# Kernel tuning notes

Measured on AMD Instinct MI355X. Metric: run time of the kernel, lower is better.

## Reference

```python
import jax, jax.numpy as jnp
import numpy as np
import math

B, S, D_MODEL, H, CLIP = 4, 1024, 1024, 16, 16
HEAD_DIM = D_MODEL // H
NEG = -1e6


def setup_inputs() -> dict:
    key = jax.random.key(0)
    ks = jax.random.split(key, 10)
    scale = 1.0 / math.sqrt(D_MODEL)
    return {
        "queries": jax.random.normal(ks[0], (B, S, D_MODEL), jnp.float32),
        "keys": jax.random.normal(ks[1], (B, S, D_MODEL), jnp.float32),
        "values": jax.random.normal(ks[2], (B, S, D_MODEL), jnp.float32),
        "valid_lens": jax.random.randint(ks[3], (B,), 1, S + 1),
        "Wq": jax.random.normal(ks[4], (D_MODEL, D_MODEL), jnp.float32) * scale,
        "Wk": jax.random.normal(ks[5], (D_MODEL, D_MODEL), jnp.float32) * scale,
        "Wv": jax.random.normal(ks[6], (D_MODEL, D_MODEL), jnp.float32) * scale,
        "Wo": jax.random.normal(ks[7], (D_MODEL, D_MODEL), jnp.float32) * scale,
        "Ek": jax.random.normal(ks[8], (2 * CLIP + 1, HEAD_DIM), jnp.float32),
        "Ev": jax.random.normal(ks[9], (2 * CLIP + 1, HEAD_DIM), jnp.float32),
    }


def _split_heads(x):
    # [B, S, D] -> [B*H, S, head_dim]
    b, s, _ = x.shape
    return x.reshape(b, s, H, HEAD_DIM).transpose(0, 2, 1, 3).reshape(b * H, s, HEAD_DIM)


def reference(queries, keys, values, valid_lens, Wq, Wk, Wv, Wo, Ek, Ev):
    q = _split_heads(queries @ Wq.T)  # [BH, S, d]
    k = _split_heads(keys @ Wk.T)
    v = _split_heads(values @ Wv.T)

    # relative-position tables, shared across batch and heads: [Sq, Sk, d]
    rng = jnp.arange(S)
    dist = jnp.clip(rng[None, :] - rng[:, None], -CLIP, CLIP) + CLIP
    pos_k = Ek[dist]
    pos_v = Ev[dist]

    scores = jnp.einsum('bqd,bkd->bqk', q, k) + jnp.einsum('bqd,qkd->bqk', q, pos_k)
    scores = scores / math.sqrt(HEAD_DIM)

    vl = jnp.repeat(valid_lens, H)  # [B*H]
    mask = jnp.arange(S)[None, None, :] < vl[:, None, None]
    attn = jax.nn.softmax(jnp.where(mask, scores, NEG), axis=-1)

    out = jnp.einsum('bqk,bkd->bqd', attn, v) + jnp.einsum('bqk,qkd->bqd', attn, pos_v)

    # merge heads: [B*H, S, d] -> [B, S, D]
    out = out.reshape(B, H, S, HEAD_DIM).transpose(0, 2, 1, 3).reshape(B, S, D_MODEL)
    return out @ Wo.T
```

## Files before the change

kernel.cpp:

```cpp
#include <hip/hip_runtime.h>


typedef __attribute__((ext_vector_type(8))) short short8;
typedef __attribute__((ext_vector_type(4))) float floatx4;

__device__ __forceinline__ unsigned short f2bf(float f) {
  union { float f; unsigned u; } v; v.f = f;
  return (unsigned short)((v.u + 0x7fffu + ((v.u >> 16) & 1u)) >> 16);
}
__device__ __forceinline__ unsigned packbf(float lo, float hi) {
  return ((unsigned)f2bf(hi) << 16) | (unsigned)f2bf(lo);
}

__device__ __forceinline__ void gld16(const void* g, void* l) {
  __builtin_amdgcn_global_load_lds(
      (const __attribute__((address_space(1))) unsigned*)g,
      (__attribute__((address_space(3))) unsigned*)l, 16, 0, 0);
}

#define WS_XQ  ((size_t)0)
#define WS_XK  ((size_t)4194304)
#define WS_XV  ((size_t)8388608)
#define WS_W   ((size_t)12582912)
#define WS_EKB ((size_t)16777216)
#define WS_EVT ((size_t)16781312)
#define WS_QB  ((size_t)16785408)
#define WS_KB  ((size_t)20979712)
#define WS_VT  ((size_t)25174016)
#define WS_OB  ((size_t)0)

__global__ __launch_bounds__(256) void convert_all_kernel(
    const float* __restrict__ q, const float* __restrict__ k,
    const float* __restrict__ v,
    const float* __restrict__ wq, const float* __restrict__ wk,
    const float* __restrict__ wv, const float* __restrict__ wo,
    const float* __restrict__ Ek, const float* __restrict__ Ev,
    const int* __restrict__ valid_lens, unsigned short* __restrict__ ws) {
  int z = blockIdx.z;
  if (z < 3) {
    const float* src = z == 0 ? q : (z == 1 ? k : v);
    unsigned short* dst = ws + (size_t)z * 4194304;
    size_t i = ((size_t)blockIdx.x * 256 + threadIdx.x) * 8;
    if (z > 0) {
      int b = (int)(i >> 20), s = (int)((i >> 10) & 1023);
      if (s >= valid_lens[b]) return;
    }
    float4 a = *(const float4*)(src + i);
    float4 bb = *(const float4*)(src + i + 4);
    uint4 o = { packbf(a.x, a.y), packbf(a.z, a.w), packbf(bb.x, bb.y), packbf(bb.z, bb.w) };
    *(uint4*)(dst + i) = o;
  } else if (z < 7) {
    if (blockIdx.x >= 512) return;
    const float* src = (z == 3) ? wq : (z == 4 ? wk : (z == 5 ? wv : wo));
    unsigned short* dst = ws + WS_W + (size_t)(z - 3) * 1048576;
    size_t i = ((size_t)blockIdx.x * 256 + threadIdx.x) * 8;
    float4 a = *(const float4*)(src + i);
    float4 bb = *(const float4*)(src + i + 4);
    uint4 o = { packbf(a.x, a.y), packbf(a.z, a.w), packbf(bb.x, bb.y), packbf(bb.z, bb.w) };
    *(uint4*)(dst + i) = o;
  } else {
    if (blockIdx.x >= 4) return;
    int gid = blockIdx.x * 256 + threadIdx.x;
    unsigned short* ekb = ws + WS_EKB;
    int i0 = gid * 8;
    unsigned short vals[8];
#pragma unroll
    for (int u = 0; u < 8; u++) {
      int i = i0 + u;
      if (i < 4096) {
        int t = i >> 6, d = i & 63;
        vals[u] = (t < 33) ? f2bf(Ek[t * 64 + d]) : (unsigned short)0;
      } else {
        int j = i - 4096;
        int d = j >> 6, t = j & 63;
        vals[u] = (t < 33) ? f2bf(Ev[t * 64 + d]) : (unsigned short)0;
      }
    }
    *(uint4*)(ekb + i0) = *(uint4*)vals;
  }
}

__device__ __forceinline__ void gemm128_body(
    const unsigned short* __restrict__ A, const unsigned short* __restrict__ W,
    unsigned short* __restrict__ Cb, float* __restrict__ Cf, int mode, float scale) {
  __shared__ unsigned short sA[128 * 32];
  __shared__ unsigned short sB[128 * 32];
  const int tid = threadIdx.x, wave = tid >> 6, lane = tid & 63;
  const int lr = lane & 15, lq = lane >> 4;
  const int wr = wave >> 1, wc = wave & 1;
  const int m0 = blockIdx.y * 128, n0 = blockIdx.x * 128;
  const int srow = lane >> 2, scol = (lane & 3) * 8;

  const unsigned short* gA0 = A + (size_t)(m0 + wave * 16 + srow) * 1024 + scol;
  const unsigned short* gA1 = gA0 + (size_t)64 * 1024;
  const unsigned short* gB0 = W + (size_t)(n0 + wave * 16 + srow) * 1024 + scol;
  const unsigned short* gB1 = gB0 + (size_t)64 * 1024;
  unsigned short* lA0 = sA + wave * 512;  unsigned short* lA1 = lA0 + 2048;
  unsigned short* lB0 = sB + wave * 512;  unsigned short* lB1 = lB0 + 2048;

  floatx4 acc[4][4];
#pragma unroll
  for (int mi = 0; mi < 4; mi++)
#pragma unroll
    for (int ni = 0; ni < 4; ni++) acc[mi][ni] = (floatx4){0.f, 0.f, 0.f, 0.f};

  for (int k0 = 0; k0 < 1024; k0 += 32) {
    gld16(gA0 + k0, lA0); gld16(gA1 + k0, lA1);
    gld16(gB0 + k0, lB0); gld16(gB1 + k0, lB1);
    __syncthreads();
    short8 af[4], bf[4];
#pragma unroll
    for (int mi = 0; mi < 4; mi++)
      af[mi] = *(const short8*)(sA + (wr * 64 + mi * 16 + lr) * 32 + lq * 8);
#pragma unroll
    for (int ni = 0; ni < 4; ni++)
      bf[ni] = *(const short8*)(sB + (wc * 64 + ni * 16 + lr) * 32 + lq * 8);
#pragma unroll
    for (int mi = 0; mi < 4; mi++)
#pragma unroll
      for (int ni = 0; ni < 4; ni++)
        acc[mi][ni] = __builtin_amdgcn_mfma_f32_16x16x32_bf16(af[mi], bf[ni], acc[mi][ni], 0, 0, 0);
    __syncthreads();
  }

  if (mode == 2) {
#pragma unroll
    for (int mi = 0; mi < 4; mi++)
#pragma unroll
      for (int ni = 0; ni < 4; ni++) {
        int col = n0 + wc * 64 + ni * 16 + lr;
        int h = col >> 6, d = col & 63;
        int rowg = m0 + wr * 64 + mi * 16 + lq * 4;
        int b = rowg >> 10, s = rowg & 1023;
        uint2 pk;
        pk.x = packbf(acc[mi][ni][0], acc[mi][ni][1]);
        pk.y = packbf(acc[mi][ni][2], acc[mi][ni][3]);
        *(uint2*)(Cb + ((size_t)((b * 16 + h) * 64 + d) << 10) + s) = pk;
      }
  } else if (mode == 3) {
#pragma unroll
    for (int mi = 0; mi < 4; mi++)
#pragma unroll
      for (int ni = 0; ni < 4; ni++)
#pragma unroll
        for (int r = 0; r < 4; r++) {
          int row = m0 + wr * 64 + mi * 16 + lq * 4 + r;
          int col = n0 + wc * 64 + ni * 16 + lr;
          Cf[(size_t)row * 1024 + col] = acc[mi][ni][r];
        }
  } else {
#pragma unroll
    for (int mi = 0; mi < 4; mi++)
#pragma unroll
      for (int ni = 0; ni < 4; ni++)
#pragma unroll
        for (int r = 0; r < 4; r++) {
          int row = m0 + wr * 64 + mi * 16 + lq * 4 + r;
          int col = n0 + wc * 64 + ni * 16 + lr;
          Cb[(size_t)row * 1024 + col] = f2bf(acc[mi][ni][r] * scale);
        }
  }
}

__global__ __launch_bounds__(256, 3) void proj_qkv_kernel(
    unsigned short* __restrict__ ws, const int* __restrict__ valid_lens) {
  int z = blockIdx.z;
  if (z > 0) {
    int m0 = blockIdx.y * 128;
    if ((m0 & 1023) >= valid_lens[m0 >> 10]) return;
  }
  const unsigned short* A = ws + (size_t)z * 4194304;
  const unsigned short* W = ws + WS_W + (size_t)z * 1048576;
  unsigned short* Cb = (z == 0) ? ws + WS_QB : (z == 1 ? ws + WS_KB : ws + WS_VT);
  int mode = (z == 2) ? 2 : (z == 0 ? 0 : 1);
  float scale = (z == 0) ? 0.125f : 1.0f;
  gemm128_body(A, W, Cb, nullptr, mode, scale);
}

__global__ __launch_bounds__(256, 3) void out_proj_kernel(
    const unsigned short* __restrict__ Ob, const unsigned short* __restrict__ Wo,
    float* __restrict__ out) {
  gemm128_body(Ob, Wo, nullptr, out, 3, 1.f);
}

__global__ __launch_bounds__(64, 3) void attn_rpr_kernel(
    const unsigned short* __restrict__ Qb, const unsigned short* __restrict__ Kb,
    const unsigned short* __restrict__ Vt, const int* __restrict__ valid_lens,
    const unsigned short* __restrict__ Ekb, const unsigned short* __restrict__ Evtb,
    unsigned short* __restrict__ Ob) {
  __shared__ unsigned short sP[16 * 72];
  __shared__ float sQE[16 * 34];
  __shared__ float sW[16 * 34];

  const int lane = threadIdx.x;
  const int lr = lane & 15, lq = lane >> 4;
  const int qx = blockIdx.x, bh = blockIdx.y;
  const int b = bh >> 4;
  const int vlen = valid_lens[b];
  const int i0 = qx * 16;
  const int colh = (bh & 15) * 64;
  const size_t bat = (size_t)b * 1024 * 1024;
  const int rbase = lq * 4;

  for (int i = lane; i < 16 * 34; i += 64) sW[i] = 0.f;

  const unsigned short* gQ = Qb + bat + (size_t)(i0 + lr) * 1024 + colh + lq * 8;
  short8 aq0 = *(const short8*)(gQ);
  short8 aq1 = *(const short8*)(gQ + 32);

#pragma unroll
  for (int ni = 0; ni < 3; ni++) {
    floatx4 aqe = (floatx4){0.f, 0.f, 0.f, 0.f};
    short8 be0 = *(const short8*)(Ekb + (ni * 16 + lr) * 64 + lq * 8);
    short8 be1 = *(const short8*)(Ekb + (ni * 16 + lr) * 64 + 32 + lq * 8);
    aqe = __builtin_amdgcn_mfma_f32_16x16x32_bf16(aq0, be0, aqe, 0, 0, 0);
    aqe = __builtin_amdgcn_mfma_f32_16x16x32_bf16(aq1, be1, aqe, 0, 0, 0);
    int t = ni * 16 + lr;
    if (t < 33)
#pragma unroll
      for (int r = 0; r < 4; r++) sQE[(rbase + r) * 34 + t] = aqe[r];
  }

  floatx4 acc_o[4];
#pragma unroll
  for (int nd = 0; nd < 4; nd++) acc_o[nd] = (floatx4){0.f, 0.f, 0.f, 0.f};
  float rs0[4] = {0.f, 0.f, 0.f, 0.f};
  float rs32[4] = {0.f, 0.f, 0.f, 0.f};

  const int vcl = vlen < 1024 ? vlen : 1024;
  const int kt_max = (vcl + 63) >> 6;

  const unsigned short* gK = Kb + bat + colh;
  const unsigned short* gV = Vt + ((size_t)bh * 64) * 1024;

  for (int kt = 0; kt < kt_max; kt++) {
    const int j0 = kt * 64;

    short8 bk[4][2], bv[4][2];
#pragma unroll
    for (int ni = 0; ni < 4; ni++) {
      const unsigned short* p = gK + (size_t)(j0 + ni * 16 + lr) * 1024 + lq * 8;
      bk[ni][0] = *(const short8*)(p);
      bk[ni][1] = *(const short8*)(p + 32);
    }
#pragma unroll
    for (int nd = 0; nd < 4; nd++) {
      const unsigned short* p = gV + (size_t)(nd * 16 + lr) * 1024 + j0 + lq * 8;
      bv[nd][0] = *(const short8*)(p);
      bv[nd][1] = *(const short8*)(p + 32);
    }

    floatx4 accs[4];
#pragma unroll
    for (int ni = 0; ni < 4; ni++) {
      accs[ni] = (floatx4){0.f, 0.f, 0.f, 0.f};
      accs[ni] = __builtin_amdgcn_mfma_f32_16x16x32_bf16(aq0, bk[ni][0], accs[ni], 0, 0, 0);
      accs[ni] = __builtin_amdgcn_mfma_f32_16x16x32_bf16(aq1, bk[ni][1], accs[ni], 0, 0, 0);
    }

    const bool general = (j0 > i0 - 79) && (j0 < i0 + 31);
    if (!general) {
      const bool hi = (j0 >= i0 + 31);
      const int tconst = hi ? 32 : 0;
      float qe[4];
#pragma unroll
      for (int r = 0; r < 4; r++) qe[r] = sQE[(rbase + r) * 34 + tconst];
#pragma unroll
      for (int ni = 0; ni < 4; ni++)
#pragma unroll
        for (int r = 0; r < 4; r++) {
          int j_g = j0 + ni * 16 + lr;
          float pv = (j_g < vlen) ? __expf(accs[ni][r] + qe[r]) : 0.f;
          if (hi) rs32[r] += pv; else rs0[r] += pv;
          sP[(rbase + r) * 72 + ni * 16 + lr] = f2bf(pv);
        }
    } else {
#pragma unroll
      for (int ni = 0; ni < 4; ni++)
#pragma unroll
        for (int r = 0; r < 4; r++) {
          int i_g = i0 + rbase + r;
          int j_g = j0 + ni * 16 + lr;
          int dd = j_g - i_g; dd = dd < -16 ? -16 : (dd > 16 ? 16 : dd);
          int t = dd + 16;
          float pv = (j_g < vlen) ? __expf(accs[ni][r] + sQE[(rbase + r) * 34 + t]) : 0.f;
          atomicAdd(&sW[(rbase + r) * 34 + t], pv);
          sP[(rbase + r) * 72 + ni * 16 + lr] = f2bf(pv);
        }
    }

    short8 ap0 = *(const short8*)(sP + lr * 72 + lq * 8);
    short8 ap1 = *(const short8*)(sP + lr * 72 + 32 + lq * 8);
#pragma unroll
    for (int nd = 0; nd < 4; nd++) {
      acc_o[nd] = __builtin_amdgcn_mfma_f32_16x16x32_bf16(ap0, bv[nd][0], acc_o[nd], 0, 0, 0);
      acc_o[nd] = __builtin_amdgcn_mfma_f32_16x16x32_bf16(ap1, bv[nd][1], acc_o[nd], 0, 0, 0);
    }
  }

#pragma unroll
  for (int x = 1; x < 16; x <<= 1)
#pragma unroll
    for (int r = 0; r < 4; r++) {
      rs0[r] += __shfl_xor(rs0[r], x, 64);
      rs32[r] += __shfl_xor(rs32[r], x, 64);
    }
  if (lr == 0)
#pragma unroll
    for (int r = 0; r < 4; r++) {
      sW[(rbase + r) * 34 + 0] += rs0[r];
      sW[(rbase + r) * 34 + 32] += rs32[r];
    }

  {
    int row = lane >> 2;
    int c0 = (lane & 3) * 16;
    unsigned* sP32 = (unsigned*)sP;
#pragma unroll
    for (int q = 0; q < 8; q++) {
      int t0 = c0 + 2 * q, t1 = t0 + 1;
      float w0 = (t0 < 33) ? sW[row * 34 + t0] : 0.f;
      float w1 = (t1 < 33) ? sW[row * 34 + t1] : 0.f;
      sP32[row * 36 + (c0 >> 1) + q] = packbf(w0, w1);
    }
  }
  {
    short8 aw0 = *(const short8*)(sP + lr * 72 + lq * 8);
    short8 aw1 = *(const short8*)(sP + lr * 72 + 32 + lq * 8);
#pragma unroll
    for (int nd = 0; nd < 4; nd++) {
      short8 be0 = *(const short8*)(Evtb + (nd * 16 + lr) * 64 + lq * 8);
      short8 be1 = *(const short8*)(Evtb + (nd * 16 + lr) * 64 + 32 + lq * 8);
      acc_o[nd] = __builtin_amdgcn_mfma_f32_16x16x32_bf16(aw0, be0, acc_o[nd], 0, 0, 0);
      acc_o[nd] = __builtin_amdgcn_mfma_f32_16x16x32_bf16(aw1, be1, acc_o[nd], 0, 0, 0);
    }
  }

  float linv[4];
#pragma unroll
  for (int r = 0; r < 4; r++) {
    float l = 0.f;
#pragma unroll
    for (int t = 0; t < 33; t++) l += sW[(rbase + r) * 34 + t];
    linv[r] = 1.f / l;
  }
#pragma unroll
  for (int nd = 0; nd < 4; nd++)
#pragma unroll
    for (int r = 0; r < 4; r++) {
      int i_loc = rbase + r;
      Ob[bat + (size_t)(i0 + i_loc) * 1024 + colh + nd * 16 + lr] =
          f2bf(acc_o[nd][r] * linv[r]);
    }
}

extern "C" void kernel_launch(void* const* d_in, const int* in_sizes, int n_in,
                              void* d_out, int out_size, void* d_ws, size_t ws_size,
                              hipStream_t stream) {
  const float* queries = (const float*)d_in[0];
  const float* keys    = (const float*)d_in[1];
  const float* values  = (const float*)d_in[2];
  const int* valid_lens = (const int*)d_in[3];
  const float* Wq = (const float*)d_in[4];
  const float* Wk = (const float*)d_in[5];
  const float* Wv = (const float*)d_in[6];
  const float* Wo = (const float*)d_in[7];
  const float* Ek = (const float*)d_in[8];
  const float* Ev = (const float*)d_in[9];
  float* out = (float*)d_out;
  unsigned short* ws = (unsigned short*)d_ws;

  convert_all_kernel<<<dim3(2048, 1, 8), 256, 0, stream>>>(
      queries, keys, values, Wq, Wk, Wv, Wo, Ek, Ev, valid_lens, ws);
  proj_qkv_kernel<<<dim3(8, 32, 3), 256, 0, stream>>>(ws, valid_lens);
  attn_rpr_kernel<<<dim3(64, 64), 64, 0, stream>>>(
      ws + WS_QB, ws + WS_KB, ws + WS_VT, valid_lens, ws + WS_EKB, ws + WS_EVT, ws + WS_OB);
  out_proj_kernel<<<dim3(8, 32), 256, 0, stream>>>(ws + WS_OB, ws + WS_W + 3145728, out);
}
```

Baseline: 242.6 us.

## Split attention key range across blocks with atomic accumulation and combine pass

The attention kernel gets a third grid dimension that splits the key tiles into chunks of four 64-key tiles. Each block accumulates its partial unnormalized output and row-sum into fp32 workspace buffers with atomics. A new zero kernel clears those buffers first, and a new combine kernel normalizes the result and packs it to bf16 for the output projection. The batch/head mapping is also interleaved and the occupancy hint raised, to spread work across uneven valid lengths. The cost is extra global traffic: roughly 16 MB of fp32 is zeroed, written via atomics and read back, plus two extra kernel launches.

```diff
diff --git a/kernel.cpp b/kernel.cpp
--- a/kernel.cpp
+++ b/kernel.cpp
@@ -183,22 +183,39 @@
   gemm128_body(Ob, Wo, nullptr, out, 3, 1.f);
 }
 
-__global__ __launch_bounds__(64, 3) void attn_rpr_kernel(
+__global__ __launch_bounds__(256) void zero_kernel(float* __restrict__ accF,
+                                                   float* __restrict__ lT) {
+  if (blockIdx.x < 4096) {
+    size_t i = ((size_t)blockIdx.x * 256 + threadIdx.x) * 4;
+    *(float4*)(accF + i) = (float4){0.f, 0.f, 0.f, 0.f};
+  } else {
+    size_t i = ((size_t)(blockIdx.x - 4096) * 256 + threadIdx.x) * 4;
+    *(float4*)(lT + i) = (float4){0.f, 0.f, 0.f, 0.f};
+  }
+}
+
+__global__ __launch_bounds__(64, 6) void attn_rpr_kernel(
     const unsigned short* __restrict__ Qb, const unsigned short* __restrict__ Kb,
     const unsigned short* __restrict__ Vt, const int* __restrict__ valid_lens,
     const unsigned short* __restrict__ Ekb, const unsigned short* __restrict__ Evtb,
-    unsigned short* __restrict__ Ob) {
+    float* __restrict__ accF, float* __restrict__ lT) {
   __shared__ unsigned short sP[16 * 72];
   __shared__ float sQE[16 * 34];
   __shared__ float sW[16 * 34];
 
   const int lane = threadIdx.x;
   const int lr = lane & 15, lq = lane >> 4;
-  const int qx = blockIdx.x, bh = blockIdx.y;
-  const int b = bh >> 4;
+  const int qx = blockIdx.x, bhy = blockIdx.y, zz = blockIdx.z;
+  const int b = bhy & 3, h = bhy >> 2;
   const int vlen = valid_lens[b];
+  const int vcl = vlen < 1024 ? vlen : 1024;
+  const int kt_max = (vcl + 63) >> 6;
+  const int kt_lo = zz * 4;
+  if (kt_lo >= kt_max) return;
+  const int kt_hi = (kt_lo + 4 < kt_max) ? kt_lo + 4 : kt_max;
+
   const int i0 = qx * 16;
-  const int colh = (bh & 15) * 64;
+  const int colh = h * 64;
   const size_t bat = (size_t)b * 1024 * 1024;
   const int rbase = lq * 4;
 
@@ -227,13 +244,10 @@
   float rs0[4] = {0.f, 0.f, 0.f, 0.f};
   float rs32[4] = {0.f, 0.f, 0.f, 0.f};
 
-  const int vcl = vlen < 1024 ? vlen : 1024;
-  const int kt_max = (vcl + 63) >> 6;
-
   const unsigned short* gK = Kb + bat + colh;
-  const unsigned short* gV = Vt + ((size_t)bh * 64) * 1024;
-
-  for (int kt = 0; kt < kt_max; kt++) {
+  const unsigned short* gV = Vt + ((size_t)(b * 16 + h) * 64) * 1024;
+
+  for (int kt = kt_lo; kt < kt_hi; kt++) {
     const int j0 = kt * 64;
 
     short8 bk[4][2], bv[4][2];
@@ -336,22 +350,36 @@
     }
   }
 
-  float linv[4];
-#pragma unroll
-  for (int r = 0; r < 4; r++) {
-    float l = 0.f;
-#pragma unroll
-    for (int t = 0; t < 33; t++) l += sW[(rbase + r) * 34 + t];
-    linv[r] = 1.f / l;
-  }
+  if (lr == 0) {
+#pragma unroll
+    for (int r = 0; r < 4; r++) {
+      float l = 0.f;
+#pragma unroll
+      for (int t = 0; t < 33; t++) l += sW[(rbase + r) * 34 + t];
+      atomicAdd(&lT[(b * 1024 + i0 + rbase + r) * 16 + h], l);
+    }
+  }
+
 #pragma unroll
   for (int nd = 0; nd < 4; nd++)
 #pragma unroll
-    for (int r = 0; r < 4; r++) {
-      int i_loc = rbase + r;
-      Ob[bat + (size_t)(i0 + i_loc) * 1024 + colh + nd * 16 + lr] =
-          f2bf(acc_o[nd][r] * linv[r]);
-    }
+    for (int r = 0; r < 4; r++)
+      atomicAdd(&accF[bat + (size_t)(i0 + rbase + r) * 1024 + colh + nd * 16 + lr],
+                acc_o[nd][r]);
+}
+
+__global__ __launch_bounds__(256) void combine_kernel(
+    const float* __restrict__ accF, const float* __restrict__ lT,
+    unsigned short* __restrict__ Ob) {
+  size_t i = ((size_t)blockIdx.x * 256 + threadIdx.x) * 4;
+  int row = (int)(i >> 10);
+  int h = (int)((i & 1023) >> 6);
+  float linv = 1.f / lT[row * 16 + h];
+  float4 a = *(const float4*)(accF + i);
+  uint2 pk;
+  pk.x = packbf(a.x * linv, a.y * linv);
+  pk.y = packbf(a.z * linv, a.w * linv);
+  *(uint2*)(Ob + i) = pk;
 }
 
 extern "C" void kernel_launch(void* const* d_in, const int* in_sizes, int n_in,
@@ -370,10 +398,16 @@
   float* out = (float*)d_out;
   unsigned short* ws = (unsigned short*)d_ws;
 
+  float* accF = (float*)(ws + WS_XK);
+  float* lT   = (float*)(ws + WS_W);
+
   convert_all_kernel<<<dim3(2048, 1, 8), 256, 0, stream>>>(
       queries, keys, values, Wq, Wk, Wv, Wo, Ek, Ev, valid_lens, ws);
   proj_qkv_kernel<<<dim3(8, 32, 3), 256, 0, stream>>>(ws, valid_lens);
-  attn_rpr_kernel<<<dim3(64, 64), 64, 0, stream>>>(
-      ws + WS_QB, ws + WS_KB, ws + WS_VT, valid_lens, ws + WS_EKB, ws + WS_EVT, ws + WS_OB);
+  zero_kernel<<<4160, 256, 0, stream>>>(accF, lT);
+  attn_rpr_kernel<<<dim3(64, 64, 4), 64, 0, stream>>>(
+      ws + WS_QB, ws + WS_KB, ws + WS_VT, valid_lens, ws + WS_EKB, ws + WS_EVT,
+      accF, lT);
+  combine_kernel<<<4096, 256, 0, stream>>>(accF, lT, ws + WS_OB);
   out_proj_kernel<<<dim3(8, 32), 256, 0, stream>>>(ws + WS_OB, ws + WS_W + 3145728, out);
 }
```

Measured after the change: 304.0 us. 25.3% more time.
